# Optimization experiments

Measured on AMD Instinct MI355X. Metric: run time of the kernel, lower is better.

The kernel has to match this reference:

```python
import jax, jax.numpy as jnp
import numpy as np

B, S, D, E = 2, 2048, 1024, 16  # batch, cutoff (seq), dmodel, n_experts


def setup_inputs() -> dict:
    key = jax.random.key(0)
    k = jax.random.split(key, 6)
    scale = 1.0 / np.sqrt(D)
    return {
        "x": jax.random.normal(k[0], (B, S, D), dtype=jnp.float32),
        "gate": jax.random.normal(k[1], (D, E), dtype=jnp.float32) * scale,
        "W1": jax.random.normal(k[2], (E, D, D), dtype=jnp.float32) * scale,  # lin1: Linear(dmodel, dmodel*E), split per expert
        "b1": jnp.zeros((E, D), dtype=jnp.float32),
        "W2": jax.random.normal(k[3], (E, D, D), dtype=jnp.float32) * scale,  # lin2: Linear(dmodel*E, dmodel), split per expert
        "b2": jnp.zeros((D,), dtype=jnp.float32),
        "topk": 256,
    }


def reference(x, gate, W1, b1, W2, b2, topk):
    # Expert-choice gating: softmax over the token (cutoff) axis per expert.
    logits = jnp.einsum("bsd,de->bse", x, gate)            # (B, S, E)
    probs = jax.nn.softmax(logits, axis=1)                  # softmax over tokens
    # Each expert selects its top-k tokens.
    g, idx = jax.lax.top_k(jnp.swapaxes(probs, 1, 2), topk)  # (B, E, k)
    # Gather selected tokens: (B, E, k, D)
    xin = jnp.take_along_axis(x[:, None, :, :], idx[..., None], axis=2)
    # Per-expert 2-layer FFN (hidden size = dmodel, per width = dmodel*n_experts)
    h = jax.nn.relu(jnp.einsum("bekd,edf->bekf", xin, W1) + b1[None, :, None, :])
    out = jnp.einsum("bekf,efd->bekd", h, W2) + b2           # (B, E, k, D)
    weighted = out * g[..., None]
    # Scatter-add back to token positions.
    y = jnp.zeros_like(x)
    b_idx = jnp.arange(x.shape[0])[:, None, None]            # (B, 1, 1)
    y = y.at[b_idx, idx].add(weighted)
    return y
```

## Files before the change

kernel.cpp:

```cpp
#include <hip/hip_runtime.h>
#include <stdint.h>
#include <math.h>

constexpr int CB = 2;
constexpr int CS = 2048;
constexpr int CD = 1024;
constexpr int CE = 16;
constexpr int CK = 256;

typedef short bf16x8 __attribute__((ext_vector_type(8)));
typedef float f32x4 __attribute__((ext_vector_type(4)));

typedef __attribute__((address_space(1))) const unsigned int gu32;
typedef __attribute__((address_space(3))) unsigned int lu32;

__device__ __forceinline__ void async16(const void* g, void* l) {
    __builtin_amdgcn_global_load_lds((gu32*)g, (lu32*)l, 16, 0, 0);
}

__device__ inline unsigned short f2bf(float f) {
    union { float f; uint32_t u; } v; v.f = f;
    uint32_t u = v.u;
    uint32_t r = (u + 0x7FFFu + ((u >> 16) & 1u)) >> 16;
    return (unsigned short)r;
}

__global__ __launch_bounds__(256)
void logits_part_kernel(const float* __restrict__ x,
                        const float* __restrict__ gate,
                        float* __restrict__ part) {
    const int tt = blockIdx.x;
    const int dt = blockIdx.y;
    const int tid = threadIdx.x;

    __shared__ float Xs[256 * 17];

    float acc[CE];
#pragma unroll
    for (int e = 0; e < CE; e++) acc[e] = 0.0f;

    const int tokl = tid >> 2;
    const int c4 = (tid & 3) << 2;

    for (int dch = 0; dch < 4; dch++) {
        const int dbase = dt * 64 + dch * 16;
        __syncthreads();
#pragma unroll
        for (int q = 0; q < 4; q++) {
            const int tok = q * 64 + tokl;
            const f32x4 v = *(const f32x4*)(x + ((size_t)(tt * 256 + tok)) * CD + dbase + c4);
            Xs[tok * 17 + c4 + 0] = v[0];
            Xs[tok * 17 + c4 + 1] = v[1];
            Xs[tok * 17 + c4 + 2] = v[2];
            Xs[tok * 17 + c4 + 3] = v[3];
        }
        __syncthreads();
#pragma unroll
        for (int d = 0; d < 16; d++) {
            const float xv = Xs[tid * 17 + d];
            const float* gr = gate + (size_t)(dbase + d) * CE;
#pragma unroll
            for (int e = 0; e < CE; e++) acc[e] = fmaf(xv, gr[e], acc[e]);
        }
    }
    float* pr = part + ((size_t)dt * (CB * CS) + tt * 256 + tid) * CE;
#pragma unroll
    for (int e = 0; e < CE; e++) pr[e] = acc[e];
}

__global__ __launch_bounds__(256)
void logits_reduce_kernel(const float* __restrict__ part,
                          float* __restrict__ logits) {
    const int i = blockIdx.x * 256 + threadIdx.x;
    float s = 0.0f;
#pragma unroll
    for (int p = 0; p < 16; p++) s += part[(size_t)p * (CB * CS * CE) + i];
    logits[i] = s;
}

__global__ void topk_kernel(const float* __restrict__ logits,
                            int* __restrict__ idx_out,
                            float* __restrict__ g_out) {
    const int be = blockIdx.x;
    const int b = be >> 4, e = be & 15;
    const int tid = threadIdx.x;
    const int lane = tid & 63, wid = tid >> 6;

    __shared__ float redf[4];
    __shared__ int hist[256];
    __shared__ int wsum[4];
    __shared__ int sh_bin, sh_rank;
    __shared__ int scnt, eqc;
    __shared__ int eqbuf[CS];

    float lv[8], p[8];
    unsigned int uv[8];
#pragma unroll
    for (int j = 0; j < 8; j++) {
        const int s = tid + j * 256;
        lv[j] = logits[((size_t)(b * CS + s)) * CE + e];
    }
    float m = lv[0];
#pragma unroll
    for (int j = 1; j < 8; j++) m = fmaxf(m, lv[j]);
#pragma unroll
    for (int o = 32; o > 0; o >>= 1) m = fmaxf(m, __shfl_down(m, o));
    if (lane == 0) redf[wid] = m;
    __syncthreads();
    m = fmaxf(fmaxf(redf[0], redf[1]), fmaxf(redf[2], redf[3]));
    __syncthreads();
    float lsum = 0.0f;
#pragma unroll
    for (int j = 0; j < 8; j++) {
        p[j] = expf(lv[j] - m);
        uv[j] = __float_as_uint(p[j]);
        lsum += p[j];
    }
#pragma unroll
    for (int o = 32; o > 0; o >>= 1) lsum += __shfl_down(lsum, o);
    if (lane == 0) redf[wid] = lsum;
    __syncthreads();
    const float total = redf[0] + redf[1] + redf[2] + redf[3];
    const float inv_total = 1.0f / total;

    unsigned int prefix = 0;
    int kneed = CK;
    for (int pass = 0; pass < 4; pass++) {
        const int shift = 24 - 8 * pass;
        __syncthreads();
        hist[tid] = 0;
        __syncthreads();
        const unsigned int hmask = (pass == 0) ? 0u : (0xFFFFFFFFu << (shift + 8));
#pragma unroll
        for (int j = 0; j < 8; j++)
            if ((uv[j] & hmask) == prefix)
                atomicAdd(&hist[(uv[j] >> shift) & 255], 1);
        __syncthreads();
        const int own = hist[tid];
        int s = own;
#pragma unroll
        for (int o = 1; o < 64; o <<= 1) {
            int t = __shfl_down(s, o);
            if (lane + o < 64) s += t;
        }
        if (lane == 0) wsum[wid] = s;
        __syncthreads();
        int above = 0;
        for (int ww = wid + 1; ww < 4; ww++) above += wsum[ww];
        const int incl = s + above;
        if (incl >= kneed && (incl - own) < kneed) {
            sh_bin = tid;
            sh_rank = kneed - (incl - own);
        }
        __syncthreads();
        prefix |= ((unsigned int)sh_bin) << shift;
        kneed = sh_rank;
    }
    const unsigned int v = prefix;
    const int quota = kneed;

    if (tid == 0) { scnt = 0; eqc = 0; }
    __syncthreads();
#pragma unroll
    for (int j = 0; j < 8; j++) {
        const int s = tid + j * 256;
        if (uv[j] > v) {
            const int pos = atomicAdd(&scnt, 1);
            idx_out[be * CK + pos] = s;
            g_out[be * CK + pos] = p[j] * inv_total;
        } else if (uv[j] == v) {
            const int pos = atomicAdd(&eqc, 1);
            eqbuf[pos] = s;
        }
    }
    __syncthreads();
    if (tid == 0) {
        const int cgt = scnt;
        const int n = eqc;
        const float gv = __uint_as_float(v) * inv_total;
        if (n > quota) {
            for (int i = 0; i < quota; i++) {
                int mn = i;
                for (int k2 = i + 1; k2 < n; k2++)
                    if (eqbuf[k2] < eqbuf[mn]) mn = k2;
                const int t2 = eqbuf[i]; eqbuf[i] = eqbuf[mn]; eqbuf[mn] = t2;
            }
        }
        for (int i = 0; i < quota; i++) {
            idx_out[be * CK + cgt + i] = eqbuf[i];
            g_out[be * CK + cgt + i] = gv;
        }
    }
}

__global__ void gather_kernel(const float* __restrict__ x,
                              const int* __restrict__ idx_ws,
                              unsigned short* __restrict__ xinbuf) {
    const int row = blockIdx.x;
    const int be = row >> 8;
    const int b = be >> 4;
    const int tok = idx_ws[row];
    const int c0 = threadIdx.x * 4;
    const f32x4 f = *(const f32x4*)(x + ((size_t)b * CS + tok) * CD + c0);
    union { unsigned short u[4]; uint2 v; } t;
    t.u[0] = f2bf(f[0]); t.u[1] = f2bf(f[1]); t.u[2] = f2bf(f[2]); t.u[3] = f2bf(f[3]);
    *(uint2*)(xinbuf + (size_t)row * CD + c0) = t.v;
}

__global__ __launch_bounds__(256)
void wt_kernel(const float* __restrict__ W, unsigned short* __restrict__ Wt) {
    const int kt = blockIdx.x, nt = blockIdx.y, e = blockIdx.z;
    const float* src = W + (size_t)e * CD * CD;
    unsigned short* dst = Wt + (size_t)e * CD * CD;
    const int tid = threadIdx.x;
    __shared__ unsigned short T[64 * 64];

    const int kr = tid >> 4;
    const int n4 = (tid & 15) << 2;
#pragma unroll
    for (int it = 0; it < 4; it++) {
        const int k = it * 16 + kr;
        const f32x4 v = *(const f32x4*)(src + (size_t)(kt * 64 + k) * CD + nt * 64 + n4);
        const int pp = k >> 4;
        const int klo = k & 15;
#pragma unroll
        for (int i = 0; i < 4; i++) {
            const int n = n4 + i;
            T[n * 64 + ((pp ^ ((n >> 2) & 3)) << 4) + klo] = f2bf(v[i]);
        }
    }
    __syncthreads();
    const int n = tid >> 2;
    const int pp = tid & 3;
    const int sw = pp ^ ((n >> 2) & 3);
    const uint4 a = *(const uint4*)&T[n * 64 + (sw << 4)];
    const uint4 b = *(const uint4*)&T[n * 64 + (sw << 4) + 8];
    unsigned short* drow = dst + (size_t)(nt * 64 + n) * CD + kt * 64 + pp * 16;
    *(uint4*)drow = a;
    *(uint4*)(drow + 8) = b;
}

template <int PHASE>
__global__ __launch_bounds__(256, 4)
void ffn_gemm(const unsigned short* __restrict__ Ain,
              const unsigned short* __restrict__ Wt,
              const float* __restrict__ bias,
              unsigned short* __restrict__ hout,
              const int* __restrict__ idx_ws,
              const float* __restrict__ g_ws,
              float* __restrict__ y) {
    const int mtile = blockIdx.x;
    const int ntile = blockIdx.y;
    const int z = blockIdx.z;
    const int e = z >> 1, b = z & 1;
    const int be = b * 16 + e;
    const int tid = threadIdx.x;
    const int w = tid >> 6, l = tid & 63;
    const int wm = w & 1, wn = w >> 1;
    const int quad = l >> 4, lr = l & 15;

    __shared__ __align__(16) unsigned short As[2][128 * 32];
    __shared__ __align__(16) unsigned short Bs[2][64 * 32];

    f32x4 acc[4][2];
    const f32x4 zz = {0.f, 0.f, 0.f, 0.f};
#pragma unroll
    for (int mi = 0; mi < 4; mi++)
#pragma unroll
        for (int ni = 0; ni < 2; ni++) acc[mi][ni] = zz;

    const unsigned short* Abase = Ain + ((size_t)be * CK + mtile * 128) * CD;
    const unsigned short* Bbase = Wt + ((size_t)e * CD + ntile * 64) * CD;

    int ac_row[2], ac_kc[2], ac_c[2];
#pragma unroll
    for (int j = 0; j < 2; j++) {
        const int c = (w * 2 + j) * 64 + l;
        ac_c[j] = c;
        ac_row[j] = c >> 2;
        ac_kc[j] = (c & 3) ^ ((ac_row[j] >> 1) & 3);
    }
    const int bc = w * 64 + l;
    const int bc_row = bc >> 2;
    const int bc_kc = (bc & 3) ^ ((bc_row >> 1) & 3);

    const int fpos = (quad ^ ((lr >> 1) & 3)) * 8;

#pragma unroll
    for (int j = 0; j < 2; j++)
        async16(Abase + (size_t)ac_row[j] * CD + ac_kc[j] * 8, &As[0][ac_c[j] * 8]);
    async16(Bbase + (size_t)bc_row * CD + bc_kc * 8, &Bs[0][bc * 8]);

    for (int ks = 0; ks < 32; ks++) {
        const int cur = ks & 1;
        if (ks < 31) {
            const int nxt = cur ^ 1;
            const int k1 = (ks + 1) * 32;
#pragma unroll
            for (int j = 0; j < 2; j++)
                async16(Abase + (size_t)ac_row[j] * CD + k1 + ac_kc[j] * 8,
                        &As[nxt][ac_c[j] * 8]);
            async16(Bbase + (size_t)bc_row * CD + k1 + bc_kc * 8, &Bs[nxt][bc * 8]);
            asm volatile("s_waitcnt vmcnt(3)" ::: "memory");
        } else {
            asm volatile("s_waitcnt vmcnt(0)" ::: "memory");
        }
        asm volatile("s_barrier" ::: "memory");

        bf16x8 af[4], bfr[2];
#pragma unroll
        for (int mi = 0; mi < 4; mi++)
            af[mi] = *(const bf16x8*)&As[cur][(wm * 64 + mi * 16 + lr) * 32 + fpos];
#pragma unroll
        for (int ni = 0; ni < 2; ni++)
            bfr[ni] = *(const bf16x8*)&Bs[cur][(wn * 32 + ni * 16 + lr) * 32 + fpos];
#pragma unroll
        for (int mi = 0; mi < 4; mi++)
#pragma unroll
            for (int ni = 0; ni < 2; ni++)
                acc[mi][ni] = __builtin_amdgcn_mfma_f32_16x16x32_bf16(
                    af[mi], bfr[ni], acc[mi][ni], 0, 0, 0);

        asm volatile("s_barrier" ::: "memory");
    }

    const int gn_base = ntile * 64 + wn * 32;
    if (PHASE == 0) {
#pragma unroll
        for (int mi = 0; mi < 4; mi++)
#pragma unroll
            for (int r = 0; r < 4; r++) {
                const int slot = mtile * 128 + wm * 64 + mi * 16 + quad * 4 + r;
                unsigned short* outrow = hout + ((size_t)be * CK + slot) * CD;
#pragma unroll
                for (int ni = 0; ni < 2; ni++) {
                    const int col = gn_base + ni * 16 + lr;
                    float hv = acc[mi][ni][r] + bias[e * CD + col];
                    hv = fmaxf(hv, 0.0f);
                    outrow[col] = f2bf(hv);
                }
            }
    } else {
#pragma unroll
        for (int mi = 0; mi < 4; mi++)
#pragma unroll
            for (int r = 0; r < 4; r++) {
                const int slot = mtile * 128 + wm * 64 + mi * 16 + quad * 4 + r;
                const int tok = idx_ws[be * CK + slot];
                const float gval = g_ws[be * CK + slot];
                float* yrow = y + ((size_t)b * CS + tok) * CD;
#pragma unroll
                for (int ni = 0; ni < 2; ni++) {
                    const int col = gn_base + ni * 16 + lr;
                    const float val = (acc[mi][ni][r] + bias[col]) * gval;
                    atomicAdd(&yrow[col], val);
                }
            }
    }
}

extern "C" void kernel_launch(void* const* d_in, const int* in_sizes, int n_in,
                              void* d_out, int out_size, void* d_ws, size_t ws_size,
                              hipStream_t stream) {
    const float* x    = (const float*)d_in[0];
    const float* gate = (const float*)d_in[1];
    const float* W1   = (const float*)d_in[2];
    const float* b1   = (const float*)d_in[3];
    const float* W2   = (const float*)d_in[4];
    const float* b2   = (const float*)d_in[5];
    float* y = (float*)d_out;

    char* ws = (char*)d_ws;
    float* logits = (float*)ws;
    int* idxw = (int*)(ws + 262144);
    float* gw = (float*)(ws + 294912);
    unsigned short* xinbuf = (unsigned short*)(ws + 327680);
    unsigned short* hbuf = (unsigned short*)(ws + 17104896);
    float* partbuf = (float*)(ws + 17104896);
    unsigned short* wtbuf = (unsigned short*)(ws + 33882112);

    logits_part_kernel<<<dim3(16, 16), 256, 0, stream>>>(x, gate, partbuf);
    logits_reduce_kernel<<<CB * CS * CE / 256, 256, 0, stream>>>(partbuf, logits);
    topk_kernel<<<CB * CE, 256, 0, stream>>>(logits, idxw, gw);
    gather_kernel<<<CB * CE * CK, 256, 0, stream>>>(x, idxw, xinbuf);
    wt_kernel<<<dim3(16, 16, CE), 256, 0, stream>>>(W1, wtbuf);
    hipMemsetAsync(d_out, 0, (size_t)CB * CS * CD * sizeof(float), stream);
    ffn_gemm<0><<<dim3(2, 16, CB * CE), 256, 0, stream>>>(xinbuf, wtbuf, b1, hbuf, idxw, gw, y);
    wt_kernel<<<dim3(16, 16, CE), 256, 0, stream>>>(W2, wtbuf);
    ffn_gemm<1><<<dim3(2, 16, CB * CE), 256, 0, stream>>>(hbuf, wtbuf, b2, nullptr, idxw, gw, y);
}
```

Before: 299.4 us.

## Triple-buffer FFN GEMM LDS loads and remap block ids for expert locality

Replaces the double-buffered global-to-LDS pipeline in the FFN GEMM with a three-stage ring that prefetches two k-steps ahead, with the wait counts adjusted to match. LDS fragment reads now go through explicit ds_read_b128 inline asm followed by a single lgkmcnt wait. The 3D grid becomes a flat 1D grid whose index is decoded so that consecutive blocks cover different experts and batches, which changes how blocks spread across XCDs and L2. The extra stage raises LDS use per block, which may reduce occupancy.

```diff
diff --git a/kernel.cpp b/kernel.cpp
--- a/kernel.cpp
+++ b/kernel.cpp
@@ -13,9 +13,16 @@
 
 typedef __attribute__((address_space(1))) const unsigned int gu32;
 typedef __attribute__((address_space(3))) unsigned int lu32;
-
-__device__ __forceinline__ void async16(const void* g, void* l) {
+typedef __attribute__((address_space(3))) unsigned short lds_us;
+
+__device__ __forceinline__ void async16(const void* g, lds_us* l) {
     __builtin_amdgcn_global_load_lds((gu32*)g, (lu32*)l, 16, 0, 0);
+}
+
+__device__ __forceinline__ bf16x8 ds_read128(const lds_us* p) {
+    bf16x8 v;
+    asm volatile("ds_read_b128 %0, %1" : "=v"(v) : "v"(p));
+    return v;
 }
 
 __device__ inline unsigned short f2bf(float f) {
@@ -249,18 +256,19 @@
               const int* __restrict__ idx_ws,
               const float* __restrict__ g_ws,
               float* __restrict__ y) {
-    const int mtile = blockIdx.x;
-    const int ntile = blockIdx.y;
-    const int z = blockIdx.z;
-    const int e = z >> 1, b = z & 1;
+    const int id = blockIdx.x;
+    const int e = (id & 7) | (((id >> 3) & 1) << 3);
+    const int b = (id >> 4) & 1;
+    const int mtile = (id >> 5) & 1;
+    const int ntile = id >> 6;
     const int be = b * 16 + e;
     const int tid = threadIdx.x;
     const int w = tid >> 6, l = tid & 63;
     const int wm = w & 1, wn = w >> 1;
     const int quad = l >> 4, lr = l & 15;
 
-    __shared__ __align__(16) unsigned short As[2][128 * 32];
-    __shared__ __align__(16) unsigned short Bs[2][64 * 32];
+    __shared__ __align__(16) unsigned short As_s[3][128 * 32];
+    __shared__ __align__(16) unsigned short Bs_s[3][64 * 32];
 
     f32x4 acc[4][2];
     const f32x4 zz = {0.f, 0.f, 0.f, 0.f};
@@ -272,35 +280,40 @@
     const unsigned short* Abase = Ain + ((size_t)be * CK + mtile * 128) * CD;
     const unsigned short* Bbase = Wt + ((size_t)e * CD + ntile * 64) * CD;
 
-    int ac_row[2], ac_kc[2], ac_c[2];
+    int ac_c[2];
+    size_t ag[2];
 #pragma unroll
     for (int j = 0; j < 2; j++) {
         const int c = (w * 2 + j) * 64 + l;
         ac_c[j] = c;
-        ac_row[j] = c >> 2;
-        ac_kc[j] = (c & 3) ^ ((ac_row[j] >> 1) & 3);
+        const int row = c >> 2;
+        const int kc = (c & 3) ^ ((row >> 1) & 3);
+        ag[j] = (size_t)row * CD + kc * 8;
     }
     const int bc = w * 64 + l;
-    const int bc_row = bc >> 2;
-    const int bc_kc = (bc & 3) ^ ((bc_row >> 1) & 3);
+    const int brow = bc >> 2;
+    const size_t bg = (size_t)brow * CD + ((bc & 3) ^ ((brow >> 1) & 3)) * 8;
 
     const int fpos = (quad ^ ((lr >> 1) & 3)) * 8;
 
-#pragma unroll
-    for (int j = 0; j < 2; j++)
-        async16(Abase + (size_t)ac_row[j] * CD + ac_kc[j] * 8, &As[0][ac_c[j] * 8]);
-    async16(Bbase + (size_t)bc_row * CD + bc_kc * 8, &Bs[0][bc * 8]);
+    lds_us* pa0 = (lds_us*)As_s[0]; lds_us* pa1 = (lds_us*)As_s[1]; lds_us* pa2 = (lds_us*)As_s[2];
+    lds_us* pb0 = (lds_us*)Bs_s[0]; lds_us* pb1 = (lds_us*)Bs_s[1]; lds_us* pb2 = (lds_us*)Bs_s[2];
+
+#pragma unroll
+    for (int j = 0; j < 2; j++) async16(Abase + ag[j], pa0 + ac_c[j] * 8);
+    async16(Bbase + bg, pb0 + bc * 8);
+#pragma unroll
+    for (int j = 0; j < 2; j++) async16(Abase + ag[j] + 32, pa1 + ac_c[j] * 8);
+    async16(Bbase + bg + 32, pb1 + bc * 8);
 
     for (int ks = 0; ks < 32; ks++) {
-        const int cur = ks & 1;
-        if (ks < 31) {
-            const int nxt = cur ^ 1;
-            const int k1 = (ks + 1) * 32;
-#pragma unroll
-            for (int j = 0; j < 2; j++)
-                async16(Abase + (size_t)ac_row[j] * CD + k1 + ac_kc[j] * 8,
-                        &As[nxt][ac_c[j] * 8]);
-            async16(Bbase + (size_t)bc_row * CD + k1 + bc_kc * 8, &Bs[nxt][bc * 8]);
+        if (ks < 30) {
+            const int k2 = (ks + 2) * 32;
+#pragma unroll
+            for (int j = 0; j < 2; j++) async16(Abase + ag[j] + k2, pa2 + ac_c[j] * 8);
+            async16(Bbase + bg + k2, pb2 + bc * 8);
+            asm volatile("s_waitcnt vmcnt(6)" ::: "memory");
+        } else if (ks == 30) {
             asm volatile("s_waitcnt vmcnt(3)" ::: "memory");
         } else {
             asm volatile("s_waitcnt vmcnt(0)" ::: "memory");
@@ -310,10 +323,14 @@
         bf16x8 af[4], bfr[2];
 #pragma unroll
         for (int mi = 0; mi < 4; mi++)
-            af[mi] = *(const bf16x8*)&As[cur][(wm * 64 + mi * 16 + lr) * 32 + fpos];
+            af[mi] = ds_read128(pa0 + (wm * 64 + mi * 16 + lr) * 32 + fpos);
 #pragma unroll
         for (int ni = 0; ni < 2; ni++)
-            bfr[ni] = *(const bf16x8*)&Bs[cur][(wn * 32 + ni * 16 + lr) * 32 + fpos];
+            bfr[ni] = ds_read128(pb0 + (wn * 32 + ni * 16 + lr) * 32 + fpos);
+        asm volatile("s_waitcnt lgkmcnt(0)"
+                     : "+v"(af[0]), "+v"(af[1]), "+v"(af[2]), "+v"(af[3]),
+                       "+v"(bfr[0]), "+v"(bfr[1])
+                     :: "memory");
 #pragma unroll
         for (int mi = 0; mi < 4; mi++)
 #pragma unroll
@@ -322,6 +339,8 @@
                     af[mi], bfr[ni], acc[mi][ni], 0, 0, 0);
 
         asm volatile("s_barrier" ::: "memory");
+        lds_us* t = pa0; pa0 = pa1; pa1 = pa2; pa2 = t;
+        t = pb0; pb0 = pb1; pb1 = pb2; pb2 = t;
     }
 
     const int gn_base = ntile * 64 + wn * 32;
@@ -385,7 +404,7 @@
     gather_kernel<<<CB * CE * CK, 256, 0, stream>>>(x, idxw, xinbuf);
     wt_kernel<<<dim3(16, 16, CE), 256, 0, stream>>>(W1, wtbuf);
     hipMemsetAsync(d_out, 0, (size_t)CB * CS * CD * sizeof(float), stream);
-    ffn_gemm<0><<<dim3(2, 16, CB * CE), 256, 0, stream>>>(xinbuf, wtbuf, b1, hbuf, idxw, gw, y);
+    ffn_gemm<0><<<1024, 256, 0, stream>>>(xinbuf, wtbuf, b1, hbuf, idxw, gw, y);
     wt_kernel<<<dim3(16, 16, CE), 256, 0, stream>>>(W2, wtbuf);
-    ffn_gemm<1><<<dim3(2, 16, CB * CE), 256, 0, stream>>>(hbuf, wtbuf, b2, nullptr, idxw, gw, y);
-}
+    ffn_gemm<1><<<1024, 256, 0, stream>>>(hbuf, wtbuf, b2, nullptr, idxw, gw, y);
+}
```

Result: faster. 285.7 us (-4.6%).
